# Kernel tuning notes

Hardware: AMD Instinct MI355X
Metric: run time of the kernel (lower is better)

## Reference

```python
import jax, jax.numpy as jnp
import numpy as np

B, P, D_IN, D_MOD, N_HEADS = 512, 64, 64, 256, 4

def _ln(x, g, b):
    m = x.mean(-1, keepdims=True)
    v = ((x - m) ** 2).mean(-1, keepdims=True)
    return (x - m) / jnp.sqrt(v + 1e-5) * g + b

def _lin(x, w, b):
    return x @ w.T + b

def _mha(q, k, v, in_w, in_b, out_w, out_b, n_heads):
    # Faithful to torch nn.MultiheadAttention(batch_first=False): dim0=seq, dim1=batch.
    S, N, E = q.shape
    dh = E // n_heads
    wq, wk, wv = jnp.split(in_w, 3, axis=0)
    bq, bk, bv = jnp.split(in_b, 3)
    qp = _lin(q, wq, bq).reshape(S, N, n_heads, dh)
    kp = _lin(k, wk, bk).reshape(S, N, n_heads, dh)
    vp = _lin(v, wv, bv).reshape(S, N, n_heads, dh)
    scores = jnp.einsum('snhd,tnhd->nhst', qp, kp) * (1.0 / np.sqrt(dh))
    attn = jax.nn.softmax(scores, axis=-1)
    o = jnp.einsum('nhst,tnhd->snhd', attn, vp).reshape(S, N, E)
    return _lin(o, out_w, out_b)

def _forward(x, emb_w, emb_b, emb_g, emb_beta, post_w, post_b, post_g, post_beta,
             attn_qw, attn_qb, attn_kw, attn_kb, attn_vw, attn_vb,
             attn_inw, attn_inb, attn_outw, attn_outb, attn_g, attn_beta,
             player_w, player_b, player_g, player_beta,
             team_w, team_b, team_g, team_beta,
             pre_w, pre_b, pre_g, pre_beta, lnf_g, lnf_b, pred_w, pred_b):
    # embedding: LinearWithLayerNorm = LayerNorm(Linear(x))
    p = _ln(_lin(x, emb_w, emb_b), emb_g, emb_beta)
    # post_embedding: ResidualLinearWithLayerNorm = LayerNorm(Linear(x)) + x
    p = _ln(_lin(p, post_w, post_b), post_g, post_beta) + p
    for i in range(2):
        res = p
        q = _lin(p, attn_qw[i], attn_qb[i])
        k = _lin(p, attn_kw[i], attn_kb[i])
        v = _lin(p, attn_vw[i], attn_vb[i])
        a = _mha(q, k, v, attn_inw[i], attn_inb[i], attn_outw[i], attn_outb[i], N_HEADS)
        p = _ln(a, attn_g[i], attn_beta[i]) + res
    for i in range(2):
        p = _ln(_lin(p, player_w[i], player_b[i]), player_g[i], player_beta[i]) + p
    # segment reduce: padded-ragged scatter + sum == masked sum over the player axis.
    # NOTE: original code computes BOTH masks as original[:,:,-1]==1 (bug preserved).
    mask = (x[:, :, -1] == 1).astype(p.dtype)  # [B, P]
    home = jnp.einsum('bpd,bp->bd', p, mask)
    away = home
    teams = jnp.concatenate([home, away], axis=1)  # [B, 2*d_mod]
    for i in range(2):
        teams = _ln(_lin(teams, team_w[i], team_b[i]), team_g[i], team_beta[i]) + teams
    o = _ln(_lin(teams, pre_w, pre_b), pre_g, pre_beta)
    o = _ln(o, lnf_g, lnf_b)
    o = _lin(o, pred_w, pred_b)[:, 0]  # squeeze(dim=1)
    return o


def setup_inputs() -> dict:
    key = jax.random.key(0)
    ks = iter(jax.random.split(key, 64))
    def nrm(shape):
        return jax.random.normal(next(ks), shape, jnp.float32) * 0.02
    x = jax.random.normal(next(ks), (B, P, D_IN), jnp.float32)
    flag = jax.random.bernoulli(next(ks), 0.5, (B, P)).astype(jnp.float32)
    x = x.at[:, :, -1].set(flag)  # binary home-team indicator channel
    d, d2 = D_MOD, 2 * D_MOD
    return dict(
        x=x,
        emb_w=nrm((d, D_IN)), emb_b=jnp.zeros(d), emb_g=jnp.ones(d), emb_beta=jnp.zeros(d),
        post_w=nrm((d, d)), post_b=jnp.zeros(d), post_g=jnp.ones(d), post_beta=jnp.zeros(d),
        attn_qw=nrm((2, d, d)), attn_qb=jnp.zeros((2, d)),
        attn_kw=nrm((2, d, d)), attn_kb=jnp.zeros((2, d)),
        attn_vw=nrm((2, d, d)), attn_vb=jnp.zeros((2, d)),
        attn_inw=nrm((2, 3 * d, d)), attn_inb=jnp.zeros((2, 3 * d)),
        attn_outw=nrm((2, d, d)), attn_outb=jnp.zeros((2, d)),
        attn_g=jnp.ones((2, d)), attn_beta=jnp.zeros((2, d)),
        player_w=nrm((2, d, d)), player_b=jnp.zeros((2, d)),
        player_g=jnp.ones((2, d)), player_beta=jnp.zeros((2, d)),
        team_w=nrm((2, d2, d2)), team_b=jnp.zeros((2, d2)),
        team_g=jnp.ones((2, d2)), team_beta=jnp.zeros((2, d2)),
        pre_w=nrm((d, d2)), pre_b=jnp.zeros(d), pre_g=jnp.ones(d), pre_beta=jnp.zeros(d),
        lnf_g=jnp.ones(d), lnf_b=jnp.zeros(d),
        pred_w=nrm((1, d)), pred_b=jnp.zeros(1),
    )


def reference(x, emb_w, emb_b, emb_g, emb_beta, post_w, post_b, post_g, post_beta,
              attn_qw, attn_qb, attn_kw, attn_kb, attn_vw, attn_vb,
              attn_inw, attn_inb, attn_outw, attn_outb, attn_g, attn_beta,
              player_w, player_b, player_g, player_beta,
              team_w, team_b, team_g, team_beta,
              pre_w, pre_b, pre_g, pre_beta, lnf_g, lnf_b, pred_w, pred_b):
    return _forward(x, emb_w, emb_b, emb_g, emb_beta, post_w, post_b, post_g, post_beta,
                    attn_qw, attn_qb, attn_kw, attn_kb, attn_vw, attn_vb,
                    attn_inw, attn_inb, attn_outw, attn_outb, attn_g, attn_beta,
                    player_w, player_b, player_g, player_beta,
                    team_w, team_b, team_g, team_beta,
                    pre_w, pre_b, pre_g, pre_beta, lnf_g, lnf_b, pred_w, pred_b)
```

## Files before the change

kernel.cpp:

```cpp
#include <hip/hip_runtime.h>
#include <math.h>


typedef __bf16 bf16x8 __attribute__((ext_vector_type(8)));
typedef __bf16 bf16x4 __attribute__((ext_vector_type(4)));
typedef __bf16 bf16x2 __attribute__((ext_vector_type(2)));
typedef float  f32x4  __attribute__((ext_vector_type(4)));
typedef unsigned short u16;
typedef unsigned short u16x8 __attribute__((ext_vector_type(8)));

__device__ __forceinline__ u16 f2b(float f) {
    unsigned int u = __builtin_bit_cast(unsigned int, f);
    return (u16)((u + 0x7fffu + ((u >> 16) & 1u)) >> 16);
}
__device__ __forceinline__ float b2f(u16 u) {
    unsigned int v = ((unsigned int)u) << 16;
    return __builtin_bit_cast(float, v);
}
__device__ __forceinline__ bf16x8 ld2x64(const u16* p) {
    bf16x4 lo = *(const bf16x4*)p;
    bf16x4 hi = *(const bf16x4*)(p + 4);
    return __builtin_shufflevector(lo, hi, 0, 1, 2, 3, 4, 5, 6, 7);
}
__device__ __forceinline__ bf16x8 ld4x32(const u16* p) {
    bf16x2 a = *(const bf16x2*)p,     b = *(const bf16x2*)(p + 2);
    bf16x2 c = *(const bf16x2*)(p + 4), d = *(const bf16x2*)(p + 6);
    bf16x4 lo = __builtin_shufflevector(a, b, 0, 1, 2, 3);
    bf16x4 hi = __builtin_shufflevector(c, d, 0, 1, 2, 3);
    return __builtin_shufflevector(lo, hi, 0, 1, 2, 3, 4, 5, 6, 7);
}
__device__ __forceinline__ void split8(const float* __restrict__ s,
                                       bf16x8& hi, bf16x8& lo) {
    u16x8 h, l;
    #pragma unroll
    for (int j = 0; j < 8; ++j) {
        float v  = s[j];
        u16  hb  = f2b(v);
        h[j] = hb;
        l[j] = f2b(v - b2f(hb));
    }
    hi = __builtin_bit_cast(bf16x8, h);
    lo = __builtin_bit_cast(bf16x8, l);
}

template<int IN, bool LN, bool RES, bool AF32, int OMODE>
__device__ __forceinline__
void gemm_body(const void* __restrict__ Xa, const void* __restrict__ Xb, int ldX,
               const u16* __restrict__ Whi, const u16* __restrict__ Wlo,
               const float* __restrict__ bias,
               const float* __restrict__ g, const float* __restrict__ beta,
               const u16* __restrict__ resh, const u16* __restrict__ resl,
               int ldRes, void* __restrict__ Y0, void* __restrict__ Y1, int ldY,
               u16* __restrict__ Wb)
{
    constexpr int KT = IN / 32;
    const int tid = threadIdx.x;
    const int wv = tid >> 6, lane = tid & 63;
    const int quad = lane >> 4, l16 = lane & 15;
    const long arow = (long)blockIdx.x * 64 + wv * 16 + l16;

    const u16* sbase[8];
    int sdst[8];
    #pragma unroll
    for (int i = 0; i < 8; ++i) {
        int cid = tid + i * 256;
        int plane = cid >> 10, nt = (cid >> 6) & 15, slot = cid & 63;
        int q = slot >> 4, c = slot & 15;
        sbase[i] = (plane ? Wlo : Whi) + (long)(nt * 16 + c) * IN + q * 8;
        sdst[i]  = (plane * 16 + nt) * 512 + slot * 8;
    }
    u16x8 wreg[8];
    auto issueW = [&](int kt) {
        #pragma unroll
        for (int i = 0; i < 8; ++i) wreg[i] = *(const u16x8*)(sbase[i] + kt * 32);
    };
    auto commitW = [&](int buf) {
        #pragma unroll
        for (int i = 0; i < 8; ++i)
            *(u16x8*)&Wb[buf * 16384 + sdst[i]] = wreg[i];
    };

    bf16x8 ah[3], al[3];
    auto loadA = [&](int kt) {
        int s = kt % 3;
        long aofs = arow * (long)ldX + kt * 32 + quad * 8;
        if constexpr (AF32) {
            float av[8];
            *(f32x4*)&av[0] = *(const f32x4*)&((const float*)Xa)[aofs];
            *(f32x4*)&av[4] = *(const f32x4*)&((const float*)Xa)[aofs + 4];
            split8(av, ah[s], al[s]);
        } else {
            ah[s] = *(const bf16x8*)&((const u16*)Xa)[aofs];
            al[s] = *(const bf16x8*)&((const u16*)Xb)[aofs];
        }
    };

    f32x4 acc[16];
    #pragma unroll
    for (int nt = 0; nt < 16; ++nt) acc[nt] = f32x4{0.f, 0.f, 0.f, 0.f};

    issueW(0);
    commitW(0);
    if (KT > 1) issueW(1);
    loadA(0);
    if (KT > 1) loadA(1);
    __syncthreads();

    #pragma unroll
    for (int kt = 0; kt < KT; ++kt) {
        if (kt + 2 < KT) loadA(kt + 2);
        const u16* wb = Wb + (kt & 1) * 16384;
        const int s = kt % 3;
        #pragma unroll
        for (int nt = 0; nt < 16; ++nt) {
            bf16x8 bhi = *(const bf16x8*)&wb[nt * 512 + lane * 8];
            bf16x8 blo = *(const bf16x8*)&wb[(16 + nt) * 512 + lane * 8];
            acc[nt] = __builtin_amdgcn_mfma_f32_16x16x32_bf16(al[s], bhi, acc[nt], 0, 0, 0);
            acc[nt] = __builtin_amdgcn_mfma_f32_16x16x32_bf16(ah[s], blo, acc[nt], 0, 0, 0);
            acc[nt] = __builtin_amdgcn_mfma_f32_16x16x32_bf16(ah[s], bhi, acc[nt], 0, 0, 0);
        }
        if (kt + 1 < KT) {
            commitW((kt + 1) & 1);
            if (kt + 2 < KT) issueW(kt + 2);
            __syncthreads();
        }
    }

    #pragma unroll
    for (int nt = 0; nt < 16; ++nt) {
        float bc = bias[nt * 16 + l16];
        #pragma unroll
        for (int r = 0; r < 4; ++r) acc[nt][r] += bc;
    }

    float mean[4], rstd[4];
    if constexpr (LN) {
        float s1[4] = {0, 0, 0, 0}, s2[4] = {0, 0, 0, 0};
        #pragma unroll
        for (int nt = 0; nt < 16; ++nt)
            #pragma unroll
            for (int r = 0; r < 4; ++r) {
                s1[r] += acc[nt][r];
                s2[r] += acc[nt][r] * acc[nt][r];
            }
        #pragma unroll
        for (int off = 1; off < 16; off <<= 1)
            #pragma unroll
            for (int r = 0; r < 4; ++r) {
                s1[r] += __shfl_xor(s1[r], off, 64);
                s2[r] += __shfl_xor(s2[r], off, 64);
            }
        #pragma unroll
        for (int r = 0; r < 4; ++r) {
            mean[r] = s1[r] * (1.0f / 256.f);
            float var = s2[r] * (1.0f / 256.f) - mean[r] * mean[r];
            rstd[r] = rsqrtf(var + 1e-5f);
        }
    }
    #pragma unroll
    for (int nt = 0; nt < 16; ++nt) {
        int col = nt * 16 + l16;
        float gc = 1.f, bc2 = 0.f;
        if constexpr (LN) { gc = g[col]; bc2 = beta[col]; }
        #pragma unroll
        for (int r = 0; r < 4; ++r) {
            long row = (long)blockIdx.x * 64 + wv * 16 + quad * 4 + r;
            float v = acc[nt][r];
            if constexpr (LN) v = (v - mean[r]) * rstd[r] * gc + bc2;
            if constexpr (RES)
                v += b2f(resh[row * ldRes + col]) + b2f(resl[row * ldRes + col]);
            long yofs = row * ldY + col;
            if constexpr (OMODE == 0) {
                ((float*)Y0)[yofs] = v;
            } else if constexpr (OMODE == 1) {
                u16 hb = f2b(v);
                ((u16*)Y0)[yofs] = hb;
                ((u16*)Y1)[yofs] = f2b(v - b2f(hb));
            } else {
                ((u16*)Y0)[yofs] = f2b(v);
            }
        }
    }
}

template<int IN, bool LN, bool RES, bool AF32, int OMODE>
__global__ __launch_bounds__(256)
void gemm_kernel(const void* __restrict__ Xa, const void* __restrict__ Xb, int ldX,
                 const u16* __restrict__ Whi, const u16* __restrict__ Wlo,
                 const float* __restrict__ bias,
                 const float* __restrict__ g, const float* __restrict__ beta,
                 const u16* __restrict__ resh, const u16* __restrict__ resl,
                 int ldRes, void* __restrict__ Y0, void* __restrict__ Y1, int ldY)
{
    __shared__ u16 Wb[32768];
    gemm_body<IN, LN, RES, AF32, OMODE>(Xa, Xb, ldX, Whi, Wlo, bias, g,
                                        beta, resh, resl, ldRes, Y0, Y1,
                                        ldY, Wb);
}

__global__ __launch_bounds__(256)
void qkv_proj(const u16* __restrict__ ph, const u16* __restrict__ pl,
              const u16* __restrict__ cwL, const float* __restrict__ cb,
              u16* __restrict__ qb, u16* __restrict__ kb,
              u16* __restrict__ vh, u16* __restrict__ vl)
{
    __shared__ u16 Wb[32768];
    int wsel = blockIdx.y;
    const u16* whi = cwL + (long)wsel * 65536;
    const u16* wlo = cwL + 393216 + (long)wsel * 65536;
    const float* bias = cb + wsel * 256;
    if (wsel == 2)
        gemm_body<256, false, false, false, 1>(
            ph, pl, 256, whi, wlo, bias, nullptr, nullptr,
            nullptr, nullptr, 0, vh, vl, 256, Wb);
    else
        gemm_body<256, false, false, false, 2>(
            ph, pl, 256, whi, wlo, bias, nullptr, nullptr,
            nullptr, nullptr, 0, wsel ? (void*)kb : (void*)qb, nullptr, 256, Wb);
}

template<int IN, int OUT, bool RES>
__global__ __launch_bounds__(256)
void tail_gemm(const float* __restrict__ X,
               const u16* __restrict__ Whi, const u16* __restrict__ Wlo,
               const float* __restrict__ bias,
               const float* __restrict__ g, const float* __restrict__ beta,
               const float* __restrict__ res, float* __restrict__ Y)
{
    constexpr int NTW = OUT / 64;
    constexpr int KT  = IN / 32;
    const int tid = threadIdx.x;
    const int wv = tid >> 6, lane = tid & 63;
    const int quad = lane >> 4, l16 = lane & 15;
    const int row0 = blockIdx.x * 16;
    const int colbase = wv * (OUT / 4);

    f32x4 acc[NTW];
    #pragma unroll
    for (int nt = 0; nt < NTW; ++nt) acc[nt] = f32x4{0.f, 0.f, 0.f, 0.f};

    #pragma unroll
    for (int kt = 0; kt < KT; ++kt) {
        float av[8];
        long aofs = (long)(row0 + l16) * IN + kt * 32 + quad * 8;
        *(f32x4*)&av[0] = *(const f32x4*)&X[aofs];
        *(f32x4*)&av[4] = *(const f32x4*)&X[aofs + 4];
        bf16x8 ah, al;
        split8(av, ah, al);
        #pragma unroll
        for (int nt = 0; nt < NTW; ++nt) {
            long wofs = (long)(colbase + nt * 16 + l16) * IN + kt * 32 + quad * 8;
            bf16x8 bhi = *(const bf16x8*)&Whi[wofs];
            bf16x8 blo = *(const bf16x8*)&Wlo[wofs];
            acc[nt] = __builtin_amdgcn_mfma_f32_16x16x32_bf16(al, bhi, acc[nt], 0, 0, 0);
            acc[nt] = __builtin_amdgcn_mfma_f32_16x16x32_bf16(ah, blo, acc[nt], 0, 0, 0);
            acc[nt] = __builtin_amdgcn_mfma_f32_16x16x32_bf16(ah, bhi, acc[nt], 0, 0, 0);
        }
    }

    #pragma unroll
    for (int nt = 0; nt < NTW; ++nt) {
        float bc = bias[colbase + nt * 16 + l16];
        #pragma unroll
        for (int r = 0; r < 4; ++r) acc[nt][r] += bc;
    }

    float s1[4] = {0, 0, 0, 0}, s2[4] = {0, 0, 0, 0};
    #pragma unroll
    for (int nt = 0; nt < NTW; ++nt)
        #pragma unroll
        for (int r = 0; r < 4; ++r) {
            s1[r] += acc[nt][r];
            s2[r] += acc[nt][r] * acc[nt][r];
        }
    #pragma unroll
    for (int off = 1; off < 16; off <<= 1)
        #pragma unroll
        for (int r = 0; r < 4; ++r) {
            s1[r] += __shfl_xor(s1[r], off, 64);
            s2[r] += __shfl_xor(s2[r], off, 64);
        }
    __shared__ float r1[64], r2[64];
    if (l16 == 0) {
        #pragma unroll
        for (int r = 0; r < 4; ++r) {
            r1[wv * 16 + quad * 4 + r] = s1[r];
            r2[wv * 16 + quad * 4 + r] = s2[r];
        }
    }
    __syncthreads();
    float mean[4], rstd[4];
    #pragma unroll
    for (int r = 0; r < 4; ++r) {
        int rr = quad * 4 + r;
        float t1 = r1[rr] + r1[16 + rr] + r1[32 + rr] + r1[48 + rr];
        float t2 = r2[rr] + r2[16 + rr] + r2[32 + rr] + r2[48 + rr];
        mean[r] = t1 * (1.0f / OUT);
        float var = t2 * (1.0f / OUT) - mean[r] * mean[r];
        rstd[r] = rsqrtf(var + 1e-5f);
    }
    #pragma unroll
    for (int nt = 0; nt < NTW; ++nt) {
        int col = colbase + nt * 16 + l16;
        float gc = g[col], bc2 = beta[col];
        #pragma unroll
        for (int r = 0; r < 4; ++r) {
            int row = row0 + quad * 4 + r;
            float v = (acc[nt][r] - mean[r]) * rstd[r] * gc + bc2;
            if constexpr (RES) v += res[(long)row * OUT + col];
            Y[(long)row * OUT + col] = v;
        }
    }
}

__global__ __launch_bounds__(256)
void combine_kernel(const float* __restrict__ inw, const float* __restrict__ inb,
                    const float* __restrict__ qw, const float* __restrict__ kw,
                    const float* __restrict__ vw, const float* __restrict__ qb,
                    const float* __restrict__ kb, const float* __restrict__ vb,
                    u16* __restrict__ cw, float* __restrict__ cb)
{
    int idx = blockIdx.y, L = idx / 3, wsel = idx % 3;
    const float* Wa = inw + (long)L * 768 * 256 + wsel * 65536;
    const float* ba = inb + L * 768 + wsel * 256;
    const float* Wf = (wsel == 0 ? qw : wsel == 1 ? kw : vw) + (long)L * 65536;
    const float* bf = (wsel == 0 ? qb : wsel == 1 ? kb : vb) + L * 256;

    int o = blockIdx.x, j = threadIdx.x;
    float s = 0.f;
    for (int mm = 0; mm < 256; ++mm)
        s += Wa[o * 256 + mm] * Wf[mm * 256 + j];
    u16 hb = f2b(s);
    cw[(long)idx * 65536 + o * 256 + j] = hb;
    cw[393216 + (long)idx * 65536 + o * 256 + j] = f2b(s - b2f(hb));

    __shared__ float red[256];
    red[j] = Wa[o * 256 + j] * bf[j];
    __syncthreads();
    for (int st = 128; st > 0; st >>= 1) {
        if (j < st) red[j] += red[j + st];
        __syncthreads();
    }
    if (j == 0) cb[idx * 256 + o] = red[0] + ba[o];
}

__global__ __launch_bounds__(256)
void cast_split_multi(const float* s0, u16* d0, int n0,
                      const float* s1, u16* d1, int n1,
                      const float* s2, u16* d2, int n2,
                      const float* s3, u16* d3, int n3,
                      const float* s4, u16* d4, int n4,
                      const float* s5, u16* d5, int n5)
{
    const float* s; u16* d; int n;
    switch (blockIdx.y) {
        case 0: s = s0; d = d0; n = n0; break;
        case 1: s = s1; d = d1; n = n1; break;
        case 2: s = s2; d = d2; n = n2; break;
        case 3: s = s3; d = d3; n = n3; break;
        case 4: s = s4; d = d4; n = n4; break;
        default: s = s5; d = d5; n = n5; break;
    }
    int i = (blockIdx.x * 256 + threadIdx.x) * 4;
    if (i >= n) return;
    float4 v = *(const float4*)&s[i];
    ushort4 h, l;
    h.x = f2b(v.x); l.x = f2b(v.x - b2f(h.x));
    h.y = f2b(v.y); l.y = f2b(v.y - b2f(h.y));
    h.z = f2b(v.z); l.z = f2b(v.z - b2f(h.z));
    h.w = f2b(v.w); l.w = f2b(v.w - b2f(h.w));
    *(ushort4*)&d[i] = h;
    *(ushort4*)&d[n + i] = l;
}

#define VTS 66
#define PS  68
#define EXP2SCALE 0.18033688089184986f

__global__ __launch_bounds__(256)
void attn_kernel(const u16* __restrict__ qbuf, const u16* __restrict__ kbuf,
                 const u16* __restrict__ vh, const u16* __restrict__ vl,
                 u16* __restrict__ ofh, u16* __restrict__ ofl)
{
    const int n = blockIdx.x, h = blockIdx.y, sq = blockIdx.z;
    const int tid = threadIdx.x;
    const int wv = tid >> 6, lane = tid & 63;
    const int quad = lane >> 4, l16 = lane & 15;

    __shared__ u16 Vth[64 * VTS];
    __shared__ u16 Vtl[64 * VTS];
    __shared__ u16 Pbh[4][32 * PS];
    __shared__ u16 Pbl[4][32 * PS];

    bf16x8 qf[2][2];
    #pragma unroll
    for (int rt = 0; rt < 2; ++rt)
        #pragma unroll
        for (int kc = 0; kc < 2; ++kc) {
            long s = sq * 128 + wv * 32 + rt * 16 + l16;
            qf[rt][kc] = *(const bf16x8*)&qbuf[(s * 64 + n) * 256 + h * 64
                                               + kc * 32 + quad * 8];
        }

    f32x4 o[2][4];
    #pragma unroll
    for (int rt = 0; rt < 2; ++rt)
        #pragma unroll
        for (int dt = 0; dt < 4; ++dt) o[rt][dt] = f32x4{0.f, 0.f, 0.f, 0.f};
    float l_run[2][4] = {{0.f, 0.f, 0.f, 0.f}, {0.f, 0.f, 0.f, 0.f}};

    for (int tb = 0; tb < 8; ++tb) {
        __syncthreads();
        for (int i = tid; i < 512; i += 256) {
            int t = i >> 3, c = i & 7;
            long rofs = ((long)(tb * 64 + t) * 64 + n) * 256 + h * 64 + c * 8;
            u16x8 hvv = *(const u16x8*)&vh[rofs];
            u16x8 lvv = *(const u16x8*)&vl[rofs];
            #pragma unroll
            for (int j = 0; j < 8; ++j) {
                Vth[(c * 8 + j) * VTS + t] = hvv[j];
                Vtl[(c * 8 + j) * VTS + t] = lvv[j];
            }
        }
        __syncthreads();

        f32x4 sA[2][4];
        #pragma unroll
        for (int rt = 0; rt < 2; ++rt)
            #pragma unroll
            for (int tt = 0; tt < 4; ++tt) sA[rt][tt] = f32x4{0.f, 0.f, 0.f, 0.f};
        #pragma unroll
        for (int kc = 0; kc < 2; ++kc)
            #pragma unroll
            for (int tt = 0; tt < 4; ++tt) {
                bf16x8 kf = *(const bf16x8*)
                    &kbuf[((long)(tb * 64 + tt * 16 + l16) * 64 + n) * 256
                          + h * 64 + kc * 32 + quad * 8];
                sA[0][tt] = __builtin_amdgcn_mfma_f32_16x16x32_bf16(
                    qf[0][kc], kf, sA[0][tt], 0, 0, 0);
                sA[1][tt] = __builtin_amdgcn_mfma_f32_16x16x32_bf16(
                    qf[1][kc], kf, sA[1][tt], 0, 0, 0);
            }

        #pragma unroll
        for (int rt = 0; rt < 2; ++rt)
            #pragma unroll
            for (int r = 0; r < 4; ++r) {
                float p0 = exp2f(sA[rt][0][r] * EXP2SCALE);
                float p1 = exp2f(sA[rt][1][r] * EXP2SCALE);
                float p2 = exp2f(sA[rt][2][r] * EXP2SCALE);
                float p3 = exp2f(sA[rt][3][r] * EXP2SCALE);
                int prow = (rt * 16 + quad * 4 + r) * PS + l16;
                u16 hb;
                hb = f2b(p0); Pbh[wv][prow +  0] = hb; Pbl[wv][prow +  0] = f2b(p0 - b2f(hb));
                hb = f2b(p1); Pbh[wv][prow + 16] = hb; Pbl[wv][prow + 16] = f2b(p1 - b2f(hb));
                hb = f2b(p2); Pbh[wv][prow + 32] = hb; Pbl[wv][prow + 32] = f2b(p2 - b2f(hb));
                hb = f2b(p3); Pbh[wv][prow + 48] = hb; Pbl[wv][prow + 48] = f2b(p3 - b2f(hb));
                l_run[rt][r] += (p0 + p1) + (p2 + p3);
            }

        #pragma unroll
        for (int kc = 0; kc < 2; ++kc) {
            bf16x8 pfh[2], pfl[2];
            #pragma unroll
            for (int rt = 0; rt < 2; ++rt) {
                int pofs = (rt * 16 + l16) * PS + kc * 32 + quad * 8;
                pfh[rt] = ld2x64(&Pbh[wv][pofs]);
                pfl[rt] = ld2x64(&Pbl[wv][pofs]);
            }
            #pragma unroll
            for (int dt = 0; dt < 4; ++dt) {
                int vofs = (dt * 16 + l16) * VTS + kc * 32 + quad * 8;
                bf16x8 vfh = ld4x32(&Vth[vofs]);
                bf16x8 vfl = ld4x32(&Vtl[vofs]);
                #pragma unroll
                for (int rt = 0; rt < 2; ++rt) {
                    o[rt][dt] = __builtin_amdgcn_mfma_f32_16x16x32_bf16(
                        pfl[rt], vfh, o[rt][dt], 0, 0, 0);
                    o[rt][dt] = __builtin_amdgcn_mfma_f32_16x16x32_bf16(
                        pfh[rt], vfl, o[rt][dt], 0, 0, 0);
                    o[rt][dt] = __builtin_amdgcn_mfma_f32_16x16x32_bf16(
                        pfh[rt], vfh, o[rt][dt], 0, 0, 0);
                }
            }
        }
    }

    #pragma unroll
    for (int off = 1; off < 16; off <<= 1)
        #pragma unroll
        for (int rt = 0; rt < 2; ++rt)
            #pragma unroll
            for (int r = 0; r < 4; ++r)
                l_run[rt][r] += __shfl_xor(l_run[rt][r], off, 64);

    #pragma unroll
    for (int rt = 0; rt < 2; ++rt)
        #pragma unroll
        for (int r = 0; r < 4; ++r) {
            float inv = 1.0f / l_run[rt][r];
            long s = sq * 128 + wv * 32 + rt * 16 + quad * 4 + r;
            #pragma unroll
            for (int dt = 0; dt < 4; ++dt) {
                long idx = (s * 64 + n) * 256 + h * 64 + dt * 16 + l16;
                float val = o[rt][dt][r] * inv;
                u16 hb = f2b(val);
                ofh[idx] = hb;
                ofl[idx] = f2b(val - b2f(hb));
            }
        }
}

__global__ __launch_bounds__(256)
void team_reduce_kernel(const float* __restrict__ x, const u16* __restrict__ ph,
                        const u16* __restrict__ pl, float* __restrict__ teams)
{
    int b = blockIdx.x, d = threadIdx.x;
    float acc = 0.f;
    for (int pp = 0; pp < 64; ++pp) {
        float flag = x[((long)b * 64 + pp) * 64 + 63];
        if (flag == 1.0f) {
            long idx = ((long)b * 64 + pp) * 256 + d;
            acc += b2f(ph[idx]) + b2f(pl[idx]);
        }
    }
    teams[(long)b * 512 + d]       = acc;
    teams[(long)b * 512 + 256 + d] = acc;
}

__global__ __launch_bounds__(64)
void ln_kernel(const float* __restrict__ X, const float* __restrict__ g,
               const float* __restrict__ b, float* __restrict__ Y)
{
    int row = blockIdx.x, lane = threadIdx.x;
    float4 v = *(const float4*)&X[(long)row * 256 + lane * 4];
    float s1 = v.x + v.y + v.z + v.w;
    float s2 = v.x*v.x + v.y*v.y + v.z*v.z + v.w*v.w;
    #pragma unroll
    for (int off = 32; off > 0; off >>= 1) {
        s1 += __shfl_xor(s1, off, 64);
        s2 += __shfl_xor(s2, off, 64);
    }
    float mean = s1 * (1.f / 256.f);
    float rstd = rsqrtf(s2 * (1.f / 256.f) - mean * mean + 1e-5f);
    float4 gg = *(const float4*)&g[lane * 4];
    float4 bb = *(const float4*)&b[lane * 4];
    float4 o;
    o.x = (v.x - mean) * rstd * gg.x + bb.x;
    o.y = (v.y - mean) * rstd * gg.y + bb.y;
    o.z = (v.z - mean) * rstd * gg.z + bb.z;
    o.w = (v.w - mean) * rstd * gg.w + bb.w;
    *(float4*)&Y[(long)row * 256 + lane * 4] = o;
}

__global__ __launch_bounds__(64)
void pred_kernel(const float* __restrict__ X, const float* __restrict__ pw,
                 const float* __restrict__ pb, float* __restrict__ out)
{
    int row = blockIdx.x, lane = threadIdx.x;
    float4 v = *(const float4*)&X[(long)row * 256 + lane * 4];
    float4 w = *(const float4*)&pw[lane * 4];
    float s = v.x*w.x + v.y*w.y + v.z*w.z + v.w*w.w;
    #pragma unroll
    for (int off = 32; off > 0; off >>= 1) s += __shfl_xor(s, off, 64);
    if (lane == 0) out[row] = s + pb[0];
}

extern "C" void kernel_launch(void* const* d_in, const int* in_sizes, int n_in,
                              void* d_out, int out_size, void* d_ws, size_t ws_size,
                              hipStream_t stream)
{
    const float* x         = (const float*)d_in[0];
    const float* emb_w     = (const float*)d_in[1];
    const float* emb_b     = (const float*)d_in[2];
    const float* emb_g     = (const float*)d_in[3];
    const float* emb_beta  = (const float*)d_in[4];
    const float* post_w    = (const float*)d_in[5];
    const float* post_b    = (const float*)d_in[6];
    const float* post_g    = (const float*)d_in[7];
    const float* post_beta = (const float*)d_in[8];
    const float* attn_qw   = (const float*)d_in[9];
    const float* attn_qb   = (const float*)d_in[10];
    const float* attn_kw   = (const float*)d_in[11];
    const float* attn_kb   = (const float*)d_in[12];
    const float* attn_vw   = (const float*)d_in[13];
    const float* attn_vb   = (const float*)d_in[14];
    const float* attn_inw  = (const float*)d_in[15];
    const float* attn_inb  = (const float*)d_in[16];
    const float* attn_outw = (const float*)d_in[17];
    const float* attn_outb = (const float*)d_in[18];
    const float* attn_g    = (const float*)d_in[19];
    const float* attn_beta = (const float*)d_in[20];
    const float* player_w  = (const float*)d_in[21];
    const float* player_b  = (const float*)d_in[22];
    const float* player_g  = (const float*)d_in[23];
    const float* player_bt = (const float*)d_in[24];
    const float* team_w    = (const float*)d_in[25];
    const float* team_b    = (const float*)d_in[26];
    const float* team_g    = (const float*)d_in[27];
    const float* team_beta = (const float*)d_in[28];
    const float* pre_w     = (const float*)d_in[29];
    const float* pre_b     = (const float*)d_in[30];
    const float* pre_g     = (const float*)d_in[31];
    const float* pre_beta  = (const float*)d_in[32];
    const float* lnf_g     = (const float*)d_in[33];
    const float* lnf_b     = (const float*)d_in[34];
    const float* pred_w    = (const float*)d_in[35];
    const float* pred_b    = (const float*)d_in[36];

    char* base = (char*)d_ws;
    const size_t NR = (size_t)32768 * 256;
    u16* ph  = (u16*)base;  base += NR * 2;
    u16* pl  = (u16*)base;  base += NR * 2;
    u16* ofh = (u16*)base;  base += NR * 2;
    u16* ofl = (u16*)base;  base += NR * 2;
    u16* vh  = (u16*)base;  base += NR * 2;
    u16* vl  = (u16*)base;  base += NR * 2;
    u16* qb  = (u16*)base;  base += NR * 2;
    u16* kb  = (u16*)base;  base += NR * 2;
    float* teams0 = (float*)base; base += (size_t)512 * 512 * 4;
    float* teams1 = (float*)base; base += (size_t)512 * 512 * 4;
    float* o5     = (float*)base; base += (size_t)512 * 256 * 4;
    u16* emb_wp    = (u16*)base;  base += (size_t)2 * 16384 * 2;
    u16* post_wp   = (u16*)base;  base += (size_t)2 * 65536 * 2;
    u16* outw_p    = (u16*)base;  base += (size_t)2 * 131072 * 2;
    u16* player_wp = (u16*)base;  base += (size_t)2 * 131072 * 2;
    u16* team_wp   = (u16*)base;  base += (size_t)2 * 524288 * 2;
    u16* pre_wp    = (u16*)base;  base += (size_t)2 * 131072 * 2;
    u16* cwb       = (u16*)base;  base += (size_t)2 * 393216 * 2;
    float* cbf     = (float*)base; base += (size_t)1536 * 4;

    cast_split_multi<<<dim3(512, 6), 256, 0, stream>>>(
        emb_w, emb_wp, 16384,
        post_w, post_wp, 65536,
        attn_outw, outw_p, 131072,
        player_w, player_wp, 131072,
        team_w, team_wp, 524288,
        pre_w, pre_wp, 131072);

    combine_kernel<<<dim3(256, 6), 256, 0, stream>>>(
        attn_inw, attn_inb, attn_qw, attn_kw, attn_vw,
        attn_qb, attn_kb, attn_vb, cwb, cbf);

    gemm_kernel<64, true, false, true, 1><<<512, 256, 0, stream>>>(
        x, nullptr, 64, emb_wp, emb_wp + 16384, emb_b, emb_g, emb_beta,
        nullptr, nullptr, 0, ph, pl, 256);
    gemm_kernel<256, true, true, false, 1><<<512, 256, 0, stream>>>(
        ph, pl, 256, post_wp, post_wp + 65536, post_b, post_g, post_beta,
        ph, pl, 256, ph, pl, 256);

    for (int L = 0; L < 2; ++L) {
        qkv_proj<<<dim3(512, 3), 256, 0, stream>>>(
            ph, pl, cwb + (size_t)L * 3 * 65536, cbf + L * 768,
            qb, kb, vh, vl);
        attn_kernel<<<dim3(64, 4, 4), 256, 0, stream>>>(qb, kb, vh, vl, ofh, ofl);
        gemm_kernel<256, true, true, false, 1><<<512, 256, 0, stream>>>(
            ofh, ofl, 256, outw_p + (size_t)L * 65536,
            outw_p + 131072 + (size_t)L * 65536, attn_outb + L * 256,
            attn_g + L * 256, attn_beta + L * 256, ph, pl, 256, ph, pl, 256);
    }

    for (int L = 0; L < 2; ++L)
        gemm_kernel<256, true, true, false, 1><<<512, 256, 0, stream>>>(
            ph, pl, 256, player_wp + (size_t)L * 65536,
            player_wp + 131072 + (size_t)L * 65536, player_b + L * 256,
            player_g + L * 256, player_bt + L * 256, ph, pl, 256, ph, pl, 256);

    team_reduce_kernel<<<512, 256, 0, stream>>>(x, ph, pl, teams0);

    tail_gemm<512, 512, true><<<32, 256, 0, stream>>>(
        teams0, team_wp, team_wp + 524288, team_b,
        team_g, team_beta, teams0, teams1);
    tail_gemm<512, 512, true><<<32, 256, 0, stream>>>(
        teams1, team_wp + 262144, team_wp + 524288 + 262144, team_b + 512,
        team_g + 512, team_beta + 512, teams1, teams0);

    tail_gemm<512, 256, false><<<32, 256, 0, stream>>>(
        teams0, pre_wp, pre_wp + 131072, pre_b, pre_g, pre_beta,
        nullptr, o5);
    ln_kernel<<<512, 64, 0, stream>>>(o5, lnf_g, lnf_b, o5);
    pred_kernel<<<512, 64, 0, stream>>>(o5, pred_w, pred_b, (float*)d_out);
}
```

Before: 799.3 us.

## Write V transposed from projection and stage weights via global_load_lds

Splits the V projection into a dedicated kernel that writes V in a transposed per-batch layout, so the attention kernel can read V fragments directly from global memory instead of transposing them through shared memory with extra barriers each tile. Separately, weight staging in the GEMM bodies switches from register round-trips to direct global-to-LDS loads, with the barrier moved ahead of the next stage. This removes LDS transpose work and register pressure, at the cost of an extra kernel launch and uncached global V reads inside attention.

```diff
diff --git a/kernel.cpp b/kernel.cpp
--- a/kernel.cpp
+++ b/kernel.cpp
@@ -4,11 +4,14 @@
 
 typedef __bf16 bf16x8 __attribute__((ext_vector_type(8)));
 typedef __bf16 bf16x4 __attribute__((ext_vector_type(4)));
-typedef __bf16 bf16x2 __attribute__((ext_vector_type(2)));
 typedef float  f32x4  __attribute__((ext_vector_type(4)));
 typedef unsigned short u16;
 typedef unsigned short u16x8 __attribute__((ext_vector_type(8)));
 
+typedef __attribute__((address_space(1))) const unsigned char gas_char;
+typedef __attribute__((address_space(3))) unsigned char las_char;
+#define GLL16(g, l) __builtin_amdgcn_global_load_lds((gas_char*)(g), (las_char*)(l), 16, 0, 0)
+
 __device__ __forceinline__ u16 f2b(float f) {
     unsigned int u = __builtin_bit_cast(unsigned int, f);
     return (u16)((u + 0x7fffu + ((u >> 16) & 1u)) >> 16);
@@ -20,13 +23,6 @@
 __device__ __forceinline__ bf16x8 ld2x64(const u16* p) {
     bf16x4 lo = *(const bf16x4*)p;
     bf16x4 hi = *(const bf16x4*)(p + 4);
-    return __builtin_shufflevector(lo, hi, 0, 1, 2, 3, 4, 5, 6, 7);
-}
-__device__ __forceinline__ bf16x8 ld4x32(const u16* p) {
-    bf16x2 a = *(const bf16x2*)p,     b = *(const bf16x2*)(p + 2);
-    bf16x2 c = *(const bf16x2*)(p + 4), d = *(const bf16x2*)(p + 6);
-    bf16x4 lo = __builtin_shufflevector(a, b, 0, 1, 2, 3);
-    bf16x4 hi = __builtin_shufflevector(c, d, 0, 1, 2, 3);
     return __builtin_shufflevector(lo, hi, 0, 1, 2, 3, 4, 5, 6, 7);
 }
 __device__ __forceinline__ void split8(const float* __restrict__ s,
@@ -60,24 +56,18 @@
     const long arow = (long)blockIdx.x * 64 + wv * 16 + l16;
 
     const u16* sbase[8];
-    int sdst[8];
     #pragma unroll
     for (int i = 0; i < 8; ++i) {
         int cid = tid + i * 256;
         int plane = cid >> 10, nt = (cid >> 6) & 15, slot = cid & 63;
         int q = slot >> 4, c = slot & 15;
         sbase[i] = (plane ? Wlo : Whi) + (long)(nt * 16 + c) * IN + q * 8;
-        sdst[i]  = (plane * 16 + nt) * 512 + slot * 8;
-    }
-    u16x8 wreg[8];
-    auto issueW = [&](int kt) {
-        #pragma unroll
-        for (int i = 0; i < 8; ++i) wreg[i] = *(const u16x8*)(sbase[i] + kt * 32);
-    };
-    auto commitW = [&](int buf) {
+    }
+    auto stageW = [&](int kt, int buf) {
         #pragma unroll
         for (int i = 0; i < 8; ++i)
-            *(u16x8*)&Wb[buf * 16384 + sdst[i]] = wreg[i];
+            GLL16(sbase[i] + kt * 32,
+                  (unsigned char*)Wb + buf * 32768 + (tid + i * 256) * 16);
     };
 
     bf16x8 ah[3], al[3];
@@ -99,9 +89,8 @@
     #pragma unroll
     for (int nt = 0; nt < 16; ++nt) acc[nt] = f32x4{0.f, 0.f, 0.f, 0.f};
 
-    issueW(0);
-    commitW(0);
-    if (KT > 1) issueW(1);
+    stageW(0, 0);
+    if (KT > 1) stageW(1, 1);
     loadA(0);
     if (KT > 1) loadA(1);
     __syncthreads();
@@ -120,9 +109,8 @@
             acc[nt] = __builtin_amdgcn_mfma_f32_16x16x32_bf16(ah[s], bhi, acc[nt], 0, 0, 0);
         }
         if (kt + 1 < KT) {
-            commitW((kt + 1) & 1);
-            if (kt + 2 < KT) issueW(kt + 2);
             __syncthreads();
+            if (kt + 2 < KT) stageW(kt + 2, kt & 1);
         }
     }
 
@@ -201,115 +189,94 @@
 __global__ __launch_bounds__(256)
 void qkv_proj(const u16* __restrict__ ph, const u16* __restrict__ pl,
               const u16* __restrict__ cwL, const float* __restrict__ cb,
-              u16* __restrict__ qb, u16* __restrict__ kb,
-              u16* __restrict__ vh, u16* __restrict__ vl)
+              u16* __restrict__ qb, u16* __restrict__ kb)
 {
     __shared__ u16 Wb[32768];
     int wsel = blockIdx.y;
     const u16* whi = cwL + (long)wsel * 65536;
     const u16* wlo = cwL + 393216 + (long)wsel * 65536;
-    const float* bias = cb + wsel * 256;
-    if (wsel == 2)
-        gemm_body<256, false, false, false, 1>(
-            ph, pl, 256, whi, wlo, bias, nullptr, nullptr,
-            nullptr, nullptr, 0, vh, vl, 256, Wb);
-    else
-        gemm_body<256, false, false, false, 2>(
-            ph, pl, 256, whi, wlo, bias, nullptr, nullptr,
-            nullptr, nullptr, 0, wsel ? (void*)kb : (void*)qb, nullptr, 256, Wb);
-}
-
-template<int IN, int OUT, bool RES>
+    gemm_body<256, false, false, false, 2>(
+        ph, pl, 256, whi, wlo, cb + wsel * 256, nullptr, nullptr,
+        nullptr, nullptr, 0, wsel ? (void*)kb : (void*)qb, nullptr, 256, Wb);
+}
+
 __global__ __launch_bounds__(256)
-void tail_gemm(const float* __restrict__ X,
-               const u16* __restrict__ Whi, const u16* __restrict__ Wlo,
-               const float* __restrict__ bias,
-               const float* __restrict__ g, const float* __restrict__ beta,
-               const float* __restrict__ res, float* __restrict__ Y)
-{
-    constexpr int NTW = OUT / 64;
-    constexpr int KT  = IN / 32;
+void v_proj(const u16* __restrict__ ph, const u16* __restrict__ pl,
+            const u16* __restrict__ whi, const u16* __restrict__ wlo,
+            const float* __restrict__ bias,
+            u16* __restrict__ vth, u16* __restrict__ vtl)
+{
+    __shared__ u16 Wb[32768];
+    constexpr int IN = 256, KT = 8;
     const int tid = threadIdx.x;
     const int wv = tid >> 6, lane = tid & 63;
     const int quad = lane >> 4, l16 = lane & 15;
-    const int row0 = blockIdx.x * 16;
-    const int colbase = wv * (OUT / 4);
-
-    f32x4 acc[NTW];
-    #pragma unroll
-    for (int nt = 0; nt < NTW; ++nt) acc[nt] = f32x4{0.f, 0.f, 0.f, 0.f};
+    const int n = blockIdx.x & 63, sblk = blockIdx.x >> 6;
+
+    const u16* sbase[8];
+    #pragma unroll
+    for (int i = 0; i < 8; ++i) {
+        int cid = tid + i * 256;
+        int plane = cid >> 10, nt = (cid >> 6) & 15, slot = cid & 63;
+        int q = slot >> 4, c = slot & 15;
+        sbase[i] = (plane ? wlo : whi) + (long)(nt * 16 + c) * IN + q * 8;
+    }
+    auto stageW = [&](int kt, int buf) {
+        #pragma unroll
+        for (int i = 0; i < 8; ++i)
+            GLL16(sbase[i] + kt * 32,
+                  (unsigned char*)Wb + buf * 32768 + (tid + i * 256) * 16);
+    };
+    const long abase = ((long)(sblk * 64 + wv * 16 + l16) * 64 + n) * 256;
+    bf16x8 ah[3], al[3];
+    auto loadA = [&](int kt) {
+        int s = kt % 3;
+        ah[s] = *(const bf16x8*)&ph[abase + kt * 32 + quad * 8];
+        al[s] = *(const bf16x8*)&pl[abase + kt * 32 + quad * 8];
+    };
+
+    f32x4 acc[16];
+    #pragma unroll
+    for (int nt = 0; nt < 16; ++nt) acc[nt] = f32x4{0.f, 0.f, 0.f, 0.f};
+
+    stageW(0, 0); stageW(1, 1);
+    loadA(0); loadA(1);
+    __syncthreads();
 
     #pragma unroll
     for (int kt = 0; kt < KT; ++kt) {
-        float av[8];
-        long aofs = (long)(row0 + l16) * IN + kt * 32 + quad * 8;
-        *(f32x4*)&av[0] = *(const f32x4*)&X[aofs];
-        *(f32x4*)&av[4] = *(const f32x4*)&X[aofs + 4];
-        bf16x8 ah, al;
-        split8(av, ah, al);
-        #pragma unroll
-        for (int nt = 0; nt < NTW; ++nt) {
-            long wofs = (long)(colbase + nt * 16 + l16) * IN + kt * 32 + quad * 8;
-            bf16x8 bhi = *(const bf16x8*)&Whi[wofs];
-            bf16x8 blo = *(const bf16x8*)&Wlo[wofs];
-            acc[nt] = __builtin_amdgcn_mfma_f32_16x16x32_bf16(al, bhi, acc[nt], 0, 0, 0);
-            acc[nt] = __builtin_amdgcn_mfma_f32_16x16x32_bf16(ah, blo, acc[nt], 0, 0, 0);
-            acc[nt] = __builtin_amdgcn_mfma_f32_16x16x32_bf16(ah, bhi, acc[nt], 0, 0, 0);
-        }
-    }
-
-    #pragma unroll
-    for (int nt = 0; nt < NTW; ++nt) {
-        float bc = bias[colbase + nt * 16 + l16];
-        #pragma unroll
-        for (int r = 0; r < 4; ++r) acc[nt][r] += bc;
-    }
-
-    float s1[4] = {0, 0, 0, 0}, s2[4] = {0, 0, 0, 0};
-    #pragma unroll
-    for (int nt = 0; nt < NTW; ++nt)
+        if (kt + 2 < KT) loadA(kt + 2);
+        const u16* wb = Wb + (kt & 1) * 16384;
+        const int s = kt % 3;
+        #pragma unroll
+        for (int nt = 0; nt < 16; ++nt) {
+            bf16x8 bhi = *(const bf16x8*)&wb[nt * 512 + lane * 8];
+            bf16x8 blo = *(const bf16x8*)&wb[(16 + nt) * 512 + lane * 8];
+            acc[nt] = __builtin_amdgcn_mfma_f32_16x16x32_bf16(al[s], bhi, acc[nt], 0, 0, 0);
+            acc[nt] = __builtin_amdgcn_mfma_f32_16x16x32_bf16(ah[s], blo, acc[nt], 0, 0, 0);
+            acc[nt] = __builtin_amdgcn_mfma_f32_16x16x32_bf16(ah[s], bhi, acc[nt], 0, 0, 0);
+        }
+        if (kt + 1 < KT) {
+            __syncthreads();
+            if (kt + 2 < KT) stageW(kt + 2, kt & 1);
+        }
+    }
+
+    #pragma unroll
+    for (int nt = 0; nt < 16; ++nt) {
+        float bc = bias[nt * 16 + l16];
+        ushort4 hv, lv;
         #pragma unroll
         for (int r = 0; r < 4; ++r) {
-            s1[r] += acc[nt][r];
-            s2[r] += acc[nt][r] * acc[nt][r];
-        }
-    #pragma unroll
-    for (int off = 1; off < 16; off <<= 1)
-        #pragma unroll
-        for (int r = 0; r < 4; ++r) {
-            s1[r] += __shfl_xor(s1[r], off, 64);
-            s2[r] += __shfl_xor(s2[r], off, 64);
-        }
-    __shared__ float r1[64], r2[64];
-    if (l16 == 0) {
-        #pragma unroll
-        for (int r = 0; r < 4; ++r) {
-            r1[wv * 16 + quad * 4 + r] = s1[r];
-            r2[wv * 16 + quad * 4 + r] = s2[r];
-        }
-    }
-    __syncthreads();
-    float mean[4], rstd[4];
-    #pragma unroll
-    for (int r = 0; r < 4; ++r) {
-        int rr = quad * 4 + r;
-        float t1 = r1[rr] + r1[16 + rr] + r1[32 + rr] + r1[48 + rr];
-        float t2 = r2[rr] + r2[16 + rr] + r2[32 + rr] + r2[48 + rr];
-        mean[r] = t1 * (1.0f / OUT);
-        float var = t2 * (1.0f / OUT) - mean[r] * mean[r];
-        rstd[r] = rsqrtf(var + 1e-5f);
-    }
-    #pragma unroll
-    for (int nt = 0; nt < NTW; ++nt) {
-        int col = colbase + nt * 16 + l16;
-        float gc = g[col], bc2 = beta[col];
-        #pragma unroll
-        for (int r = 0; r < 4; ++r) {
-            int row = row0 + quad * 4 + r;
-            float v = (acc[nt][r] - mean[r]) * rstd[r] * gc + bc2;
-            if constexpr (RES) v += res[(long)row * OUT + col];
-            Y[(long)row * OUT + col] = v;
-        }
+            float v = acc[nt][r] + bc;
+            u16 hb = f2b(v);
+            ((u16*)&hv)[r] = hb;
+            ((u16*)&lv)[r] = f2b(v - b2f(hb));
+        }
+        long ofs = ((long)n * 256 + nt * 16 + l16) * 512
+                 + sblk * 64 + wv * 16 + quad * 4;
+        *(ushort4*)&vth[ofs] = hv;
+        *(ushort4*)&vtl[ofs] = lv;
     }
 }
 
@@ -373,13 +340,12 @@
     *(ushort4*)&d[n + i] = l;
 }
 
-#define VTS 66
 #define PS  68
 #define EXP2SCALE 0.18033688089184986f
 
 __global__ __launch_bounds__(256)
 void attn_kernel(const u16* __restrict__ qbuf, const u16* __restrict__ kbuf,
-                 const u16* __restrict__ vh, const u16* __restrict__ vl,
+                 const u16* __restrict__ vth, const u16* __restrict__ vtl,
                  u16* __restrict__ ofh, u16* __restrict__ ofl)
 {
     const int n = blockIdx.x, h = blockIdx.y, sq = blockIdx.z;
@@ -387,8 +353,6 @@
     const int wv = tid >> 6, lane = tid & 63;
     const int quad = lane >> 4, l16 = lane & 15;
 
-    __shared__ u16 Vth[64 * VTS];
-    __shared__ u16 Vtl[64 * VTS];
     __shared__ u16 Pbh[4][32 * PS];
     __shared__ u16 Pbl[4][32 * PS];
 
@@ -402,6 +366,8 @@
                                                + kc * 32 + quad * 8];
         }
 
+    const long vbase = ((long)n * 256 + h * 64) * 512;
+
     f32x4 o[2][4];
     #pragma unroll
     for (int rt = 0; rt < 2; ++rt)
@@ -410,20 +376,6 @@
     float l_run[2][4] = {{0.f, 0.f, 0.f, 0.f}, {0.f, 0.f, 0.f, 0.f}};
 
     for (int tb = 0; tb < 8; ++tb) {
-        __syncthreads();
-        for (int i = tid; i < 512; i += 256) {
-            int t = i >> 3, c = i & 7;
-            long rofs = ((long)(tb * 64 + t) * 64 + n) * 256 + h * 64 + c * 8;
-            u16x8 hvv = *(const u16x8*)&vh[rofs];
-            u16x8 lvv = *(const u16x8*)&vl[rofs];
-            #pragma unroll
-            for (int j = 0; j < 8; ++j) {
-                Vth[(c * 8 + j) * VTS + t] = hvv[j];
-                Vtl[(c * 8 + j) * VTS + t] = lvv[j];
-            }
-        }
-        __syncthreads();
-
         f32x4 sA[2][4];
         #pragma unroll
         for (int rt = 0; rt < 2; ++rt)
@@ -470,9 +422,10 @@
             }
             #pragma unroll
             for (int dt = 0; dt < 4; ++dt) {
-                int vofs = (dt * 16 + l16) * VTS + kc * 32 + quad * 8;
-                bf16x8 vfh = ld4x32(&Vth[vofs]);
-                bf16x8 vfl = ld4x32(&Vtl[vofs]);
+                long vofs = vbase + (long)(dt * 16 + l16) * 512
+                          + tb * 64 + kc * 32 + quad * 8;
+                bf16x8 vfh = *(const bf16x8*)&vth[vofs];
+                bf16x8 vfl = *(const bf16x8*)&vtl[vofs];
                 #pragma unroll
                 for (int rt = 0; rt < 2; ++rt) {
                     o[rt][dt] = __builtin_amdgcn_mfma_f32_16x16x32_bf16(
@@ -526,6 +479,100 @@
     }
     teams[(long)b * 512 + d]       = acc;
     teams[(long)b * 512 + 256 + d] = acc;
+}
+
+template<int IN, int OUT, bool RES>
+__global__ __launch_bounds__(256)
+void tail_gemm(const float* __restrict__ X,
+               const u16* __restrict__ Whi, const u16* __restrict__ Wlo,
+               const float* __restrict__ bias,
+               const float* __restrict__ g, const float* __restrict__ beta,
+               const float* __restrict__ res, float* __restrict__ Y)
+{
+    constexpr int NTW = OUT / 64;
+    constexpr int KT  = IN / 32;
+    const int tid = threadIdx.x;
+    const int wv = tid >> 6, lane = tid & 63;
+    const int quad = lane >> 4, l16 = lane & 15;
+    const int row0 = blockIdx.x * 16;
+    const int colbase = wv * (OUT / 4);
+
+    f32x4 acc[NTW];
+    #pragma unroll
+    for (int nt = 0; nt < NTW; ++nt) acc[nt] = f32x4{0.f, 0.f, 0.f, 0.f};
+
+    #pragma unroll
+    for (int kt = 0; kt < KT; ++kt) {
+        float av[8];
+        long aofs = (long)(row0 + l16) * IN + kt * 32 + quad * 8;
+        *(f32x4*)&av[0] = *(const f32x4*)&X[aofs];
+        *(f32x4*)&av[4] = *(const f32x4*)&X[aofs + 4];
+        bf16x8 ah, al;
+        split8(av, ah, al);
+        #pragma unroll
+        for (int nt = 0; nt < NTW; ++nt) {
+            long wofs = (long)(colbase + nt * 16 + l16) * IN + kt * 32 + quad * 8;
+            bf16x8 bhi = *(const bf16x8*)&Whi[wofs];
+            bf16x8 blo = *(const bf16x8*)&Wlo[wofs];
+            acc[nt] = __builtin_amdgcn_mfma_f32_16x16x32_bf16(al, bhi, acc[nt], 0, 0, 0);
+            acc[nt] = __builtin_amdgcn_mfma_f32_16x16x32_bf16(ah, blo, acc[nt], 0, 0, 0);
+            acc[nt] = __builtin_amdgcn_mfma_f32_16x16x32_bf16(ah, bhi, acc[nt], 0, 0, 0);
+        }
+    }
+
+    #pragma unroll
+    for (int nt = 0; nt < NTW; ++nt) {
+        float bc = bias[colbase + nt * 16 + l16];
+        #pragma unroll
+        for (int r = 0; r < 4; ++r) acc[nt][r] += bc;
+    }
+
+    float s1[4] = {0, 0, 0, 0}, s2[4] = {0, 0, 0, 0};
+    #pragma unroll
+    for (int nt = 0; nt < NTW; ++nt)
+        #pragma unroll
+        for (int r = 0; r < 4; ++r) {
+            s1[r] += acc[nt][r];
+            s2[r] += acc[nt][r] * acc[nt][r];
+        }
+    #pragma unroll
+    for (int off = 1; off < 16; off <<= 1)
+        #pragma unroll
+        for (int r = 0; r < 4; ++r) {
+            s1[r] += __shfl_xor(s1[r], off, 64);
+            s2[r] += __shfl_xor(s2[r], off, 64);
+        }
+    __shared__ float r1[64], r2[64];
+    if (l16 == 0) {
+        #pragma unroll
+        for (int r = 0; r < 4; ++r) {
+            r1[wv * 16 + quad * 4 + r] = s1[r];
+            r2[wv * 16 + quad * 4 + r] = s2[r];
+        }
+    }
+    __syncthreads();
+    float mean[4], rstd[4];
+    #pragma unroll
+    for (int r = 0; r < 4; ++r) {
+        int rr = quad * 4 + r;
+        float t1 = r1[rr] + r1[16 + rr] + r1[32 + rr] + r1[48 + rr];
+        float t2 = r2[rr] + r2[16 + rr] + r2[32 + rr] + r2[48 + rr];
+        mean[r] = t1 * (1.0f / OUT);
+        float var = t2 * (1.0f / OUT) - mean[r] * mean[r];
+        rstd[r] = rsqrtf(var + 1e-5f);
+    }
+    #pragma unroll
+    for (int nt = 0; nt < NTW; ++nt) {
+        int col = colbase + nt * 16 + l16;
+        float gc = g[col], bc2 = beta[col];
+        #pragma unroll
+        for (int r = 0; r < 4; ++r) {
+            int row = row0 + quad * 4 + r;
+            float v = (acc[nt][r] - mean[r]) * rstd[r] * gc + bc2;
+            if constexpr (RES) v += res[(long)row * OUT + col];
+            Y[(long)row * OUT + col] = v;
+        }
+    }
 }
 
 __global__ __launch_bounds__(64)
@@ -614,8 +661,8 @@
     u16* pl  = (u16*)base;  base += NR * 2;
     u16* ofh = (u16*)base;  base += NR * 2;
     u16* ofl = (u16*)base;  base += NR * 2;
-    u16* vh  = (u16*)base;  base += NR * 2;
-    u16* vl  = (u16*)base;  base += NR * 2;
+    u16* vth = (u16*)base;  base += NR * 2;
+    u16* vtl = (u16*)base;  base += NR * 2;
     u16* qb  = (u16*)base;  base += NR * 2;
     u16* kb  = (u16*)base;  base += NR * 2;
     float* teams0 = (float*)base; base += (size_t)512 * 512 * 4;
@@ -650,10 +697,14 @@
         ph, pl, 256, ph, pl, 256);
 
     for (int L = 0; L < 2; ++L) {
-        qkv_proj<<<dim3(512, 3), 256, 0, stream>>>(
-            ph, pl, cwb + (size_t)L * 3 * 65536, cbf + L * 768,
-            qb, kb, vh, vl);
-        attn_kernel<<<dim3(64, 4, 4), 256, 0, stream>>>(qb, kb, vh, vl, ofh, ofl);
+        const u16* cwL = cwb + (size_t)L * 3 * 65536;
+        qkv_proj<<<dim3(512, 2), 256, 0, stream>>>(
+            ph, pl, cwL, cbf + L * 768, qb, kb);
+        v_proj<<<512, 256, 0, stream>>>(
+            ph, pl, cwL + 2 * 65536, cwL + 393216 + 2 * 65536,
+            cbf + L * 768 + 512, vth, vtl);
+        attn_kernel<<<dim3(64, 4, 4), 256, 0, stream>>>(
+            qb, kb, vth, vtl, ofh, ofl);
         gemm_kernel<256, true, true, false, 1><<<512, 256, 0, stream>>>(
             ofh, ofl, 256, outw_p + (size_t)L * 65536,
             outw_p + 131072 + (size_t)L * 65536, attn_outb + L * 256,
```

Result: slower. 926.3 us (+15.9%).
